# Kernel optimization log

Hardware: AMD Instinct MI355X
Metric: run time of the kernel (lower is better)

## Reference

```python
import jax, jax.numpy as jnp
import numpy as np

L, K, B = 4, 8192, 1


def _sinusoid_table(n_position, d_hid):
    # matches PositionalEncoding._get_sinusoid_encoding_table
    pos = jnp.arange(n_position, dtype=jnp.float32)[:, None]
    i = jnp.arange(d_hid)[None, :]
    angle = pos / jnp.power(jnp.float32(10000.0), (2 * (i // 2)).astype(jnp.float32) / d_hid)
    table = jnp.where(i % 2 == 0, jnp.sin(angle), jnp.cos(angle))
    return table[None]  # (1, n_position, d_hid)


def _conv2d_same(x, w, b):
    # x: (N, C_in, H, W), w: (C_out, C_in, 3, 3), 3x3 stride-1 'same' conv
    y = jax.lax.conv_general_dilated(x, w, window_strides=(1, 1), padding='SAME',
                                     dimension_numbers=('NCHW', 'OIHW', 'NCHW'))
    return y + b[None, :, None, None]


def setup_inputs() -> dict:
    key = jax.random.key(0)
    ks = jax.random.split(key, 9)
    N = K * B
    return {
        'X': jax.random.normal(ks[0], (L, N), jnp.float32),
        'S': jax.random.normal(ks[1], (L, N), jnp.float32),
        'W_1x': jax.random.normal(ks[2], (L, L), jnp.float32),
        'W_1s': jax.random.normal(ks[3], (L, L), jnp.float32),
        'W_2x': jax.random.normal(ks[4], (K, K), jnp.float32),
        'conv_wx': jax.random.normal(ks[5], (2 * L, 2 * L, 3, 3), jnp.float32) * 0.1,
        'conv_bx': jax.random.normal(ks[6], (2 * L,), jnp.float32) * 0.1,
        'conv_ws': jax.random.normal(ks[7], (2 * L, 2 * L, 3, 3), jnp.float32) * 0.1,
        'conv_bs': jax.random.normal(ks[8], (2 * L,), jnp.float32) * 0.1,
    }


def reference(X, S, W_1x, W_1s, W_2x, conv_wx, conv_bx, conv_ws, conv_bs):
    N = K * B
    Xe = W_1x @ S          # (L, N)
    Se = W_1s @ X          # (L, N)
    # rank-L attention: NxN score matrix, softmax over dim 0 (columns normalized)
    Ax = jax.nn.softmax(Xe.T @ Xe, axis=0)   # (N, N)
    As = jax.nn.softmax(Se.T @ Se, axis=0)   # (N, N)
    Xa = Xe @ Ax           # (L, N)
    Sa = Se @ As           # (L, N)
    Mx = (W_2x @ Xa.reshape(K, L * B)).reshape(L, N)
    Ms = (W_2x @ Sa.reshape(K, L * B)).reshape(L, N)
    Xm = Mx * X
    Sm = Ms * X  # faithful to source: multiplies by X, not S
    X_hat = jnp.concatenate([Xm, X], axis=0).reshape(2 * L, K, B)
    S_hat = jnp.concatenate([Sm, S], axis=0).reshape(2 * L, K, B)
    S_hat = S_hat + _sinusoid_table(K, B)    # (2L,K,B) + (1,K,B)
    X_e_hat = _conv2d_same(X_hat[None], conv_wx, conv_bx)  # (1, 2L, K, B)
    S_e_hat = _conv2d_same(S_hat[None], conv_ws, conv_bs)  # (1, 2L, K, B)
    return jnp.concatenate([X_e_hat, S_e_hat], axis=0)     # (2, 2L, K, B)
```

## Files before the change

kernel.cpp:

```cpp
#include <hip/hip_runtime.h>

#define NPOS 8192
#define NCH  16
#define CHUNK (NPOS / NCH)
#define L2E 1.4426950408889634f

#if __has_builtin(__builtin_amdgcn_exp2f)
#define EXP2F(x) __builtin_amdgcn_exp2f(x)
#else
#define EXP2F(x) __expf((x) * 0.69314718055994531f)
#endif

#define OFF_PART  0u
#define OFF_XA    1572864u
#define OFF_SA    1605632u
#define OFF_MX2A  1638400u
#define OFF_MS2A  1671168u
#define OFF_MX2B  1703936u
#define OFF_MS2B  1736704u

__global__ __launch_bounds__(256) void k_attn(
    const float* __restrict__ X, const float* __restrict__ S,
    const float* __restrict__ W1x, const float* __restrict__ W1s,
    float* __restrict__ ws)
{
    const int branch = blockIdx.z;
    const float* src = branch ? X : S;
    const float* W1  = branch ? W1s : W1x;
    float w[16];
#pragma unroll
    for (int i = 0; i < 16; ++i) w[i] = W1[i];

    __shared__ float4 tile[CHUNK];
    __shared__ float red[4];
    const int tid = threadIdx.x;
    const int i0 = blockIdx.y * CHUNK;

    float mloc = 0.f;
#pragma unroll
    for (int u0 = 0; u0 < CHUNK; u0 += 256) {
        int u = u0 + tid, i = i0 + u;
        float a0 = src[0*NPOS+i], a1 = src[1*NPOS+i];
        float a2 = src[2*NPOS+i], a3 = src[3*NPOS+i];
        float e0 = fmaf(w[ 0],a0,fmaf(w[ 1],a1,fmaf(w[ 2],a2,w[ 3]*a3)));
        float e1 = fmaf(w[ 4],a0,fmaf(w[ 5],a1,fmaf(w[ 6],a2,w[ 7]*a3)));
        float e2 = fmaf(w[ 8],a0,fmaf(w[ 9],a1,fmaf(w[10],a2,w[11]*a3)));
        float e3 = fmaf(w[12],a0,fmaf(w[13],a1,fmaf(w[14],a2,w[15]*a3)));
        tile[u] = make_float4(e0, e1, e2, e3);
        mloc = fmaxf(mloc, fmaf(e0,e0,fmaf(e1,e1,fmaf(e2,e2,e3*e3))));
    }
    for (int off = 32; off; off >>= 1) mloc = fmaxf(mloc, __shfl_down(mloc, off));
    if ((tid & 63) == 0) red[tid >> 6] = mloc;
    __syncthreads();
    float R = sqrtf(fmaxf(fmaxf(red[0], red[1]), fmaxf(red[2], red[3])));

    int j = blockIdx.x * 256 + tid;
    float b0 = src[0*NPOS+j], b1 = src[1*NPOS+j];
    float b2 = src[2*NPOS+j], b3 = src[3*NPOS+j];
    float q0 = fmaf(w[ 0],b0,fmaf(w[ 1],b1,fmaf(w[ 2],b2,w[ 3]*b3)));
    float q1 = fmaf(w[ 4],b0,fmaf(w[ 5],b1,fmaf(w[ 6],b2,w[ 7]*b3)));
    float q2 = fmaf(w[ 8],b0,fmaf(w[ 9],b1,fmaf(w[10],b2,w[11]*b3)));
    float q3 = fmaf(w[12],b0,fmaf(w[13],b1,fmaf(w[14],b2,w[15]*b3)));
    float nj = sqrtf(fmaf(q0,q0,fmaf(q1,q1,fmaf(q2,q2,q3*q3))));
    float Mj = R * nj * L2E;
    float negM = -Mj;
    float x0 = q0*L2E, x1 = q1*L2E, x2 = q2*L2E, x3 = q3*L2E;

    float den = 0.f, n0 = 0.f, n1 = 0.f, n2 = 0.f, n3 = 0.f;
#pragma unroll 4
    for (int u = 0; u < CHUNK; ++u) {
        float4 xi = tile[u];
        float s = fmaf(x0,xi.x, fmaf(x1,xi.y, fmaf(x2,xi.z, fmaf(x3,xi.w, negM))));
        float p = EXP2F(s);
        den += p;
        n0 = fmaf(p, xi.x, n0);
        n1 = fmaf(p, xi.y, n1);
        n2 = fmaf(p, xi.z, n2);
        n3 = fmaf(p, xi.w, n3);
    }
    float* part = ws + OFF_PART + (size_t)(branch * NCH + blockIdx.y) * 6 * NPOS;
    part[0*NPOS + j] = n0;
    part[1*NPOS + j] = n1;
    part[2*NPOS + j] = n2;
    part[3*NPOS + j] = n3;
    part[4*NPOS + j] = den;
    part[5*NPOS + j] = Mj;
}

__global__ __launch_bounds__(256) void k_fin(float* __restrict__ ws)
{
    int branch = blockIdx.y;
    int j = blockIdx.x * 256 + threadIdx.x;
    const float* base = ws + OFF_PART + (size_t)branch * NCH * 6 * NPOS + j;
    float M = 0.f;
#pragma unroll
    for (int c = 0; c < NCH; ++c) M = fmaxf(M, base[(size_t)(c*6+5) * NPOS]);
    float n0=0.f, n1=0.f, n2=0.f, n3=0.f, den=0.f;
#pragma unroll
    for (int c = 0; c < NCH; ++c) {
        const float* p = base + (size_t)c * 6 * NPOS;
        float wgt = EXP2F(p[5*NPOS] - M);
        n0 = fmaf(p[0*NPOS], wgt, n0);
        n1 = fmaf(p[1*NPOS], wgt, n1);
        n2 = fmaf(p[2*NPOS], wgt, n2);
        n3 = fmaf(p[3*NPOS], wgt, n3);
        den = fmaf(p[4*NPOS], wgt, den);
    }
    float inv = 1.0f / den;
    float* out = ws + (branch ? OFF_SA : OFF_XA);
    out[0*NPOS + j] = n0 * inv;
    out[1*NPOS + j] = n1 * inv;
    out[2*NPOS + j] = n2 * inv;
    out[3*NPOS + j] = n3 * inv;
}

__global__ __launch_bounds__(256, 4) void k_gemv(
    const float* __restrict__ W2, float* __restrict__ ws)
{
    __shared__ float4 lx[1024];
    __shared__ float4 lsb[1024];
    const int tid  = threadIdx.x;
    const int wave = tid >> 6, lane = tid & 63;
    const int half = blockIdx.y;
    const int r0   = blockIdx.x * 16 + wave * 4;
    const float4* xa4 = (const float4*)(ws + OFF_XA);
    const float4* sa4 = (const float4*)(ws + OFF_SA);
    const float*  wr  = W2 + (size_t)r0 * NPOS;

    float acc[4][8];
#pragma unroll
    for (int r = 0; r < 4; ++r)
#pragma unroll
        for (int c = 0; c < 8; ++c) acc[r][c] = 0.f;

    for (int ph = 0; ph < 4; ++ph) {
        const int kbase = half * 4096 + ph * 1024;
        if (ph) __syncthreads();
#pragma unroll
        for (int p = 0; p < 4; ++p) {
            int t  = p * 256 + tid;
            int sw = t ^ ((t >> 2) & 7);
            lx[sw]  = xa4[kbase + t];
            lsb[sw] = sa4[kbase + t];
        }
        __syncthreads();
#pragma unroll
        for (int s = 0; s < 4; ++s) {
            int q = s * 64 + lane;
            float4 w0 = *(const float4*)(wr + 0*NPOS + kbase + q*4);
            float4 w1 = *(const float4*)(wr + 1*NPOS + kbase + q*4);
            float4 w2v= *(const float4*)(wr + 2*NPOS + kbase + q*4);
            float4 w3 = *(const float4*)(wr + 3*NPOS + kbase + q*4);
            int ib = (4*q) ^ (q & 7);
            float4 a[4], b[4];
#pragma unroll
            for (int m = 0; m < 4; ++m) { a[m] = lx[ib ^ m]; b[m] = lsb[ib ^ m]; }
#pragma unroll
            for (int m = 0; m < 4; ++m) {
                float c0 = (m==0)?w0.x:(m==1)?w0.y:(m==2)?w0.z:w0.w;
                float c1 = (m==0)?w1.x:(m==1)?w1.y:(m==2)?w1.z:w1.w;
                float c2 = (m==0)?w2v.x:(m==1)?w2v.y:(m==2)?w2v.z:w2v.w;
                float c3 = (m==0)?w3.x:(m==1)?w3.y:(m==2)?w3.z:w3.w;
                acc[0][0]=fmaf(c0,a[m].x,acc[0][0]); acc[0][1]=fmaf(c0,a[m].y,acc[0][1]);
                acc[0][2]=fmaf(c0,a[m].z,acc[0][2]); acc[0][3]=fmaf(c0,a[m].w,acc[0][3]);
                acc[0][4]=fmaf(c0,b[m].x,acc[0][4]); acc[0][5]=fmaf(c0,b[m].y,acc[0][5]);
                acc[0][6]=fmaf(c0,b[m].z,acc[0][6]); acc[0][7]=fmaf(c0,b[m].w,acc[0][7]);
                acc[1][0]=fmaf(c1,a[m].x,acc[1][0]); acc[1][1]=fmaf(c1,a[m].y,acc[1][1]);
                acc[1][2]=fmaf(c1,a[m].z,acc[1][2]); acc[1][3]=fmaf(c1,a[m].w,acc[1][3]);
                acc[1][4]=fmaf(c1,b[m].x,acc[1][4]); acc[1][5]=fmaf(c1,b[m].y,acc[1][5]);
                acc[1][6]=fmaf(c1,b[m].z,acc[1][6]); acc[1][7]=fmaf(c1,b[m].w,acc[1][7]);
                acc[2][0]=fmaf(c2,a[m].x,acc[2][0]); acc[2][1]=fmaf(c2,a[m].y,acc[2][1]);
                acc[2][2]=fmaf(c2,a[m].z,acc[2][2]); acc[2][3]=fmaf(c2,a[m].w,acc[2][3]);
                acc[2][4]=fmaf(c2,b[m].x,acc[2][4]); acc[2][5]=fmaf(c2,b[m].y,acc[2][5]);
                acc[2][6]=fmaf(c2,b[m].z,acc[2][6]); acc[2][7]=fmaf(c2,b[m].w,acc[2][7]);
                acc[3][0]=fmaf(c3,a[m].x,acc[3][0]); acc[3][1]=fmaf(c3,a[m].y,acc[3][1]);
                acc[3][2]=fmaf(c3,a[m].z,acc[3][2]); acc[3][3]=fmaf(c3,a[m].w,acc[3][3]);
                acc[3][4]=fmaf(c3,b[m].x,acc[3][4]); acc[3][5]=fmaf(c3,b[m].y,acc[3][5]);
                acc[3][6]=fmaf(c3,b[m].z,acc[3][6]); acc[3][7]=fmaf(c3,b[m].w,acc[3][7]);
            }
        }
    }

    float* mx = ws + (half ? OFF_MX2B : OFF_MX2A);
    float* msb= ws + (half ? OFF_MS2B : OFF_MS2A);
#pragma unroll
    for (int r = 0; r < 4; ++r)
#pragma unroll
        for (int c = 0; c < 8; ++c) {
            float v = acc[r][c];
            for (int off = 32; off; off >>= 1) v += __shfl_down(v, off);
            if (lane == 0) {
                float* dst = (c < 4) ? mx : msb;
                dst[(size_t)(r0 + r) * 4 + (c & 3)] = v;
            }
        }
}

__global__ __launch_bounds__(256) void k_conv(
    const float* __restrict__ X, const float* __restrict__ S,
    const float* __restrict__ cwx, const float* __restrict__ cbx,
    const float* __restrict__ cws, const float* __restrict__ cbs,
    const float* __restrict__ ws, float* __restrict__ out)
{
    int branch = blockIdx.y;
    int k0 = blockIdx.x * 256;
    const float* M2a = ws + (branch ? OFF_MS2A : OFF_MX2A);
    const float* M2b = ws + (branch ? OFF_MS2B : OFF_MX2B);
    const float* cw = branch ? cws : cwx;
    const float* cb = branch ? cbs : cbx;

    __shared__ float h[8][264];
    __shared__ float wg[192];
    __shared__ float bg[8];

    int tid = threadIdx.x;
    if (tid < 192) {
        int co = tid / 24, rem = tid % 24, ci = rem / 3, kh = rem % 3;
        wg[tid] = cw[co * 72 + ci * 9 + kh * 3 + 1];
    }
    if (tid < 8) bg[tid] = cb[tid];

    for (int idx = tid; idx < 8 * 258; idx += 256) {
        int ch = idx / 258, kk = idx % 258;
        int k = k0 - 1 + kk;
        float v = 0.f;
        if (k >= 0 && k < NPOS) {
            int l = ch & 3;
            size_t fi = (size_t)l * NPOS + k;
            if (branch == 0) {
                float xv = X[fi];
                v = (ch < 4) ? (M2a[fi] + M2b[fi]) * xv : xv;
            } else {
                v = (ch < 4) ? (M2a[fi] + M2b[fi]) * X[fi] : S[fi];
                v += sinf((float)k);
            }
        }
        h[ch][kk] = v;
    }
    __syncthreads();

    int k = k0 + tid;
    int kk = tid + 1;
#pragma unroll
    for (int co = 0; co < 8; ++co) {
        float a = bg[co];
#pragma unroll
        for (int ci = 0; ci < 8; ++ci) {
            a = fmaf(wg[co * 24 + ci * 3 + 0], h[ci][kk - 1], a);
            a = fmaf(wg[co * 24 + ci * 3 + 1], h[ci][kk    ], a);
            a = fmaf(wg[co * 24 + ci * 3 + 2], h[ci][kk + 1], a);
        }
        out[(size_t)(branch * 8 + co) * NPOS + k] = a;
    }
}

extern "C" void kernel_launch(void* const* d_in, const int* in_sizes, int n_in,
                              void* d_out, int out_size, void* d_ws, size_t ws_size,
                              hipStream_t stream)
{
    const float* X   = (const float*)d_in[0];
    const float* S   = (const float*)d_in[1];
    const float* W1x = (const float*)d_in[2];
    const float* W1s = (const float*)d_in[3];
    const float* W2  = (const float*)d_in[4];
    const float* cwx = (const float*)d_in[5];
    const float* cbx = (const float*)d_in[6];
    const float* cws = (const float*)d_in[7];
    const float* cbs = (const float*)d_in[8];
    float* out = (float*)d_out;
    float* ws  = (float*)d_ws;

    k_attn<<<dim3(NPOS / 256, NCH, 2), 256, 0, stream>>>(X, S, W1x, W1s, ws);
    k_fin<<<dim3(NPOS / 256, 2), 256, 0, stream>>>(ws);
    k_gemv<<<dim3(NPOS / 16, 2), 256, 0, stream>>>(W2, ws);
    k_conv<<<dim3(NPOS / 256, 2), 256, 0, stream>>>(X, S, cwx, cbx, cws, cbs, ws, out);
}
```

Measured before the change: 108.5 us.

## Double-buffer GEMV shared-memory tiles with register prefetch of next chunk

Splits the k_gemv reduction into eight smaller phases, each staged through a double-buffered LDS tile. The next chunk of Xa/Sa is prefetched into registers while the current one is computed, so global-load latency can overlap with the FMAs. The FMA body is rewritten as a macro with explicit component selection. This adds an extra barrier per phase and more register pressure, which could hurt occupancy under the 4-blocks launch bound.

```diff
diff --git a/kernel.cpp b/kernel.cpp
--- a/kernel.cpp
+++ b/kernel.cpp
@@ -114,14 +114,37 @@
     out[3*NPOS + j] = n3 * inv;
 }
 
+#define GC 512
+
+#define GMADD(m, CM0, CM1, CM2, CM3)                                          \
+    {                                                                         \
+        acc[0][0]=fmaf(CM0,a[m].x,acc[0][0]); acc[0][1]=fmaf(CM0,a[m].y,acc[0][1]); \
+        acc[0][2]=fmaf(CM0,a[m].z,acc[0][2]); acc[0][3]=fmaf(CM0,a[m].w,acc[0][3]); \
+        acc[0][4]=fmaf(CM0,b[m].x,acc[0][4]); acc[0][5]=fmaf(CM0,b[m].y,acc[0][5]); \
+        acc[0][6]=fmaf(CM0,b[m].z,acc[0][6]); acc[0][7]=fmaf(CM0,b[m].w,acc[0][7]); \
+        acc[1][0]=fmaf(CM1,a[m].x,acc[1][0]); acc[1][1]=fmaf(CM1,a[m].y,acc[1][1]); \
+        acc[1][2]=fmaf(CM1,a[m].z,acc[1][2]); acc[1][3]=fmaf(CM1,a[m].w,acc[1][3]); \
+        acc[1][4]=fmaf(CM1,b[m].x,acc[1][4]); acc[1][5]=fmaf(CM1,b[m].y,acc[1][5]); \
+        acc[1][6]=fmaf(CM1,b[m].z,acc[1][6]); acc[1][7]=fmaf(CM1,b[m].w,acc[1][7]); \
+        acc[2][0]=fmaf(CM2,a[m].x,acc[2][0]); acc[2][1]=fmaf(CM2,a[m].y,acc[2][1]); \
+        acc[2][2]=fmaf(CM2,a[m].z,acc[2][2]); acc[2][3]=fmaf(CM2,a[m].w,acc[2][3]); \
+        acc[2][4]=fmaf(CM2,b[m].x,acc[2][4]); acc[2][5]=fmaf(CM2,b[m].y,acc[2][5]); \
+        acc[2][6]=fmaf(CM2,b[m].z,acc[2][6]); acc[2][7]=fmaf(CM2,b[m].w,acc[2][7]); \
+        acc[3][0]=fmaf(CM3,a[m].x,acc[3][0]); acc[3][1]=fmaf(CM3,a[m].y,acc[3][1]); \
+        acc[3][2]=fmaf(CM3,a[m].z,acc[3][2]); acc[3][3]=fmaf(CM3,a[m].w,acc[3][3]); \
+        acc[3][4]=fmaf(CM3,b[m].x,acc[3][4]); acc[3][5]=fmaf(CM3,b[m].y,acc[3][5]); \
+        acc[3][6]=fmaf(CM3,b[m].z,acc[3][6]); acc[3][7]=fmaf(CM3,b[m].w,acc[3][7]); \
+    }
+
 __global__ __launch_bounds__(256, 4) void k_gemv(
     const float* __restrict__ W2, float* __restrict__ ws)
 {
-    __shared__ float4 lx[1024];
-    __shared__ float4 lsb[1024];
+    __shared__ float4 lA[2][GC];
+    __shared__ float4 lB[2][GC];
     const int tid  = threadIdx.x;
     const int wave = tid >> 6, lane = tid & 63;
     const int half = blockIdx.y;
+    const int kb0  = half * 4096;
     const int r0   = blockIdx.x * 16 + wave * 4;
     const float4* xa4 = (const float4*)(ws + OFF_XA);
     const float4* sa4 = (const float4*)(ws + OFF_SA);
@@ -133,19 +156,38 @@
 #pragma unroll
         for (int c = 0; c < 8; ++c) acc[r][c] = 0.f;
 
-    for (int ph = 0; ph < 4; ++ph) {
-        const int kbase = half * 4096 + ph * 1024;
-        if (ph) __syncthreads();
-#pragma unroll
-        for (int p = 0; p < 4; ++p) {
+    float4 rx[2], rs[2];
+#pragma unroll
+    for (int p = 0; p < 2; ++p) {
+        int t = p * 256 + tid;
+        rx[p] = xa4[kb0 + t];
+        rs[p] = sa4[kb0 + t];
+    }
+
+    for (int ph = 0; ph < 8; ++ph) {
+        const int kbase = kb0 + ph * GC;
+        float4* dA = lA[ph & 1];
+        float4* dB = lB[ph & 1];
+#pragma unroll
+        for (int p = 0; p < 2; ++p) {
             int t  = p * 256 + tid;
             int sw = t ^ ((t >> 2) & 7);
-            lx[sw]  = xa4[kbase + t];
-            lsb[sw] = sa4[kbase + t];
+            dA[sw] = rx[p];
+            dB[sw] = rs[p];
         }
         __syncthreads();
-#pragma unroll
-        for (int s = 0; s < 4; ++s) {
+        if (ph < 7) {
+#pragma unroll
+            for (int p = 0; p < 2; ++p) {
+                int t = p * 256 + tid;
+                rx[p] = xa4[kbase + GC + t];
+                rs[p] = sa4[kbase + GC + t];
+            }
+        }
+        const float4* sA = lA[ph & 1];
+        const float4* sB = lB[ph & 1];
+#pragma unroll
+        for (int s = 0; s < 2; ++s) {
             int q = s * 64 + lane;
             float4 w0 = *(const float4*)(wr + 0*NPOS + kbase + q*4);
             float4 w1 = *(const float4*)(wr + 1*NPOS + kbase + q*4);
@@ -154,31 +196,13 @@
             int ib = (4*q) ^ (q & 7);
             float4 a[4], b[4];
 #pragma unroll
-            for (int m = 0; m < 4; ++m) { a[m] = lx[ib ^ m]; b[m] = lsb[ib ^ m]; }
-#pragma unroll
-            for (int m = 0; m < 4; ++m) {
-                float c0 = (m==0)?w0.x:(m==1)?w0.y:(m==2)?w0.z:w0.w;
-                float c1 = (m==0)?w1.x:(m==1)?w1.y:(m==2)?w1.z:w1.w;
-                float c2 = (m==0)?w2v.x:(m==1)?w2v.y:(m==2)?w2v.z:w2v.w;
-                float c3 = (m==0)?w3.x:(m==1)?w3.y:(m==2)?w3.z:w3.w;
-                acc[0][0]=fmaf(c0,a[m].x,acc[0][0]); acc[0][1]=fmaf(c0,a[m].y,acc[0][1]);
-                acc[0][2]=fmaf(c0,a[m].z,acc[0][2]); acc[0][3]=fmaf(c0,a[m].w,acc[0][3]);
-                acc[0][4]=fmaf(c0,b[m].x,acc[0][4]); acc[0][5]=fmaf(c0,b[m].y,acc[0][5]);
-                acc[0][6]=fmaf(c0,b[m].z,acc[0][6]); acc[0][7]=fmaf(c0,b[m].w,acc[0][7]);
-                acc[1][0]=fmaf(c1,a[m].x,acc[1][0]); acc[1][1]=fmaf(c1,a[m].y,acc[1][1]);
-                acc[1][2]=fmaf(c1,a[m].z,acc[1][2]); acc[1][3]=fmaf(c1,a[m].w,acc[1][3]);
-                acc[1][4]=fmaf(c1,b[m].x,acc[1][4]); acc[1][5]=fmaf(c1,b[m].y,acc[1][5]);
-                acc[1][6]=fmaf(c1,b[m].z,acc[1][6]); acc[1][7]=fmaf(c1,b[m].w,acc[1][7]);
-                acc[2][0]=fmaf(c2,a[m].x,acc[2][0]); acc[2][1]=fmaf(c2,a[m].y,acc[2][1]);
-                acc[2][2]=fmaf(c2,a[m].z,acc[2][2]); acc[2][3]=fmaf(c2,a[m].w,acc[2][3]);
-                acc[2][4]=fmaf(c2,b[m].x,acc[2][4]); acc[2][5]=fmaf(c2,b[m].y,acc[2][5]);
-                acc[2][6]=fmaf(c2,b[m].z,acc[2][6]); acc[2][7]=fmaf(c2,b[m].w,acc[2][7]);
-                acc[3][0]=fmaf(c3,a[m].x,acc[3][0]); acc[3][1]=fmaf(c3,a[m].y,acc[3][1]);
-                acc[3][2]=fmaf(c3,a[m].z,acc[3][2]); acc[3][3]=fmaf(c3,a[m].w,acc[3][3]);
-                acc[3][4]=fmaf(c3,b[m].x,acc[3][4]); acc[3][5]=fmaf(c3,b[m].y,acc[3][5]);
-                acc[3][6]=fmaf(c3,b[m].z,acc[3][6]); acc[3][7]=fmaf(c3,b[m].w,acc[3][7]);
-            }
-        }
+            for (int m = 0; m < 4; ++m) { a[m] = sA[ib ^ m]; b[m] = sB[ib ^ m]; }
+            GMADD(0, w0.x, w1.x, w2v.x, w3.x)
+            GMADD(1, w0.y, w1.y, w2v.y, w3.y)
+            GMADD(2, w0.z, w1.z, w2v.z, w3.z)
+            GMADD(3, w0.w, w1.w, w2v.w, w3.w)
+        }
+        __syncthreads();
     }
 
     float* mx = ws + (half ? OFF_MX2B : OFF_MX2A);
```

New measurement: 154.6 us. 42.5% more time.
